# Kernel tuning notes

Hardware: AMD Instinct MI355X
Metric: run time of the kernel (lower is better)

Reference implementation:

```python
import jax, jax.numpy as jnp
import numpy as np

CHAMFER_W, NORMAL_W, EDGE_W, WATERTIGHT_W, SDF_W = 1.0, 0.5, 0.3, 0.2, 1.0
DIHEDRAL_THRESHOLD = 0.5
EPS_COS = 1e-8   # F.cosine_similarity eps
EPS_NRM = 1e-12  # F.normalize eps


def _pairwise_sqdist(p, g):
    # (B,N,3),(B,M,3) -> (B,N,M) squared distances, without (B,N,M,3) temp
    p2 = (p * p).sum(-1)
    g2 = (g * g).sum(-1)
    return p2[:, :, None] + g2[:, None, :] - 2.0 * jnp.einsum('bnd,bmd->bnm', p, g)


def _face_normals(verts, faces):
    v0, v1, v2 = verts[faces[:, 0]], verts[faces[:, 1]], verts[faces[:, 2]]
    n = jnp.cross(v1 - v0, v2 - v0)
    return n / jnp.maximum(jnp.linalg.norm(n, axis=-1, keepdims=True), EPS_NRM)


def _edge_structure(faces, num_verts):
    # All 3F directed edges (f_i, f_{(i+1)%3}), canonicalized to sorted keys.
    a = faces                      # (F,3)
    b = jnp.roll(faces, -1, axis=1)  # pairs (0,1),(1,2),(2,0)
    lo = jnp.minimum(a, b).reshape(-1)
    hi = jnp.maximum(a, b).reshape(-1)
    keys = lo * num_verts + hi      # unique int key per undirected edge (< 2^31)
    face_ids = jnp.repeat(jnp.arange(faces.shape[0], dtype=jnp.int32), 3)
    order = jnp.argsort(keys, stable=True)
    sk = keys[order]
    sf = face_ids[order]
    E = sk.shape[0]
    run_start = jnp.concatenate([jnp.array([True]), sk[1:] != sk[:-1]])
    eq_next = jnp.concatenate([sk[:-1] == sk[1:], jnp.array([False])])
    rs_pad = jnp.concatenate([run_start, jnp.array([True, True])])
    # pair2[i]: run of length exactly 2 starting at i -> faces sf[i], sf[i+1]
    pair2 = run_start & eq_next & rs_pad[2:]
    return sf, pair2, run_start


def _edge_sharpness(verts, faces):
    normals = _face_normals(verts, faces)
    sf, pair2, _ = _edge_structure(faces, verts.shape[0])
    sf_next = jnp.roll(sf, -1)
    cos = (normals[sf] * normals[sf_next]).sum(-1)
    terms = jax.nn.relu(cos - DIHEDRAL_THRESHOLD)
    cnt = pair2.sum()
    return jnp.where(cnt > 0, (terms * pair2).sum() / jnp.maximum(cnt, 1), 0.0)


def _watertight(faces, num_verts):
    _, pair2, run_start = _edge_structure(faces, num_verts)
    total = run_start.sum()
    bad = total - pair2.sum()
    return jnp.where(total > 0, bad.astype(jnp.float32) / jnp.maximum(total, 1).astype(jnp.float32), 0.0)


def setup_inputs():
    key = jax.random.key(0)
    ks = jax.random.split(key, 10)
    B, N, M, V, F, NS = 1, 8192, 8192, 20000, 40000, 65536
    return {
        'pred_sdf': jax.random.normal(ks[0], (B, NS, 1), jnp.float32),
        'gt_sdf': jax.random.normal(ks[1], (B, NS, 1), jnp.float32),
        'extracted_vertices': jax.random.normal(ks[2], (V, 3), jnp.float32),
        'extracted_faces': jax.random.randint(ks[3], (F, 3), 0, V, jnp.int32),
        'gt_vertices': jax.random.normal(ks[4], (V, 3), jnp.float32),
        'gt_faces': jax.random.randint(ks[5], (F, 3), 0, V, jnp.int32),
        'pred_points': jax.random.normal(ks[6], (B, N, 3), jnp.float32),
        'gt_points': jax.random.normal(ks[7], (B, M, 3), jnp.float32),
        'pred_normals': jax.random.normal(ks[8], (B, N, 3), jnp.float32),
        'gt_normals': jax.random.normal(ks[9], (B, M, 3), jnp.float32),
    }


def reference(pred_sdf, gt_sdf, extracted_vertices, extracted_faces, gt_vertices, gt_faces,
              pred_points, gt_points, pred_normals, gt_normals):
    # sdf supervision (L1)
    sdf_l = SDF_W * jnp.abs(pred_sdf - gt_sdf).mean()

    # chamfer
    dist = _pairwise_sqdist(pred_points, gt_points)  # (B,N,M)
    min_p2g = dist.min(axis=2).mean(axis=1)
    min_g2p = dist.min(axis=1).mean(axis=1)
    chamfer_l = CHAMFER_W * (min_p2g + min_g2p).mean()

    # normal consistency (nearest GT point per pred point)
    nn_idx = jnp.argmin(dist, axis=2)  # (B,N)
    matched = jnp.take_along_axis(gt_normals, nn_idx[..., None], axis=1)  # (B,N,3)
    pn = jnp.maximum(jnp.linalg.norm(pred_normals, axis=-1), EPS_COS)
    gn = jnp.maximum(jnp.linalg.norm(matched, axis=-1), EPS_COS)
    cos = (pred_normals * matched).sum(-1) / (pn * gn)
    normal_l = NORMAL_W * (1.0 - jnp.abs(cos)).mean()

    # edge sharpness (GT mesh args are unused by the original implementation)
    edge_l = EDGE_W * _edge_sharpness(extracted_vertices, extracted_faces)

    # watertight regularization
    wt_l = WATERTIGHT_W * _watertight(extracted_faces, extracted_vertices.shape[0])

    total = sdf_l + chamfer_l + normal_l + edge_l + wt_l
    return sdf_l, chamfer_l, normal_l, edge_l, wt_l, total
```

## Files before the change

### kernel.cpp

```cpp
#include <hip/hip_runtime.h>
#include <math.h>

#define TILE 128
#define REG 8
#define APB (256 * REG)
#define HASH_C 262144
#define HASH_MASK (HASH_C - 1)
#define EMPTY_SLOT 0xFFFFFFFFu
#define KEY_MASK ((1u << 29) - 1)
#define CNT_ONE (1u << 29)
#define SDF_BLOCKS 32

#define SBIAS 256.0f
#define TOPBITS 0x42000000u
#define PADW 480.0f


__device__ inline float waveReduceF(float v) {
#pragma unroll
  for (int off = 32; off > 0; off >>= 1) v += __shfl_down(v, off, 64);
  return v;
}

__global__ __launch_bounds__(256) void fused_kernel(
    const float* __restrict__ P, const float* __restrict__ G, int N, int M,
    int p2gBlocks, int chamferBlocks, int meshBlocks, int nTileG, int nTileP,
    unsigned long long* __restrict__ p2g, unsigned* __restrict__ g2p,
    const float* __restrict__ verts, const int* __restrict__ faces, int F, int V,
    float4* __restrict__ fn, unsigned* __restrict__ slots,
    unsigned* __restrict__ face0, unsigned* __restrict__ face1,
    unsigned* __restrict__ cnt, unsigned* __restrict__ pairList,
    const float* __restrict__ sdfA, const float* __restrict__ sdfB, int NS,
    float* __restrict__ sdfPartial, float* accumF, unsigned* accumU) {
  __shared__ float4 tile[TILE];
  __shared__ float shS[4];
  int tid = threadIdx.x;

  if (blockIdx.x == 0 && tid == 0) {
#pragma unroll
    for (int q = 0; q < 5; q++) accumF[q] = 0.f;
    accumU[0] = 0u;
  }

  if ((int)blockIdx.x >= chamferBlocks + meshBlocks) {
    int sb = blockIdx.x - chamferBlocks - meshBlocks;
    int t = sb * 256 + tid;
    int strideS = SDF_BLOCKS * 256;
    float ss = 0.f;
    for (int i = t; i < NS; i += strideS) ss += fabsf(sdfA[i] - sdfB[i]);
    ss = waveReduceF(ss);
    int lane = tid & 63, wid = tid >> 6;
    if (lane == 0) shS[wid] = ss;
    __syncthreads();
    if (tid == 0) sdfPartial[sb] = shS[0] + shS[1] + shS[2] + shS[3];
    return;
  }

  if ((int)blockIdx.x >= chamferBlocks) {
    int e = (blockIdx.x - chamferBlocks) * 256 + tid;
    bool valid = (e < 3 * F);
    unsigned c = 0xFFu;
    if (valid) {
      int f = e / 3, k = e - 3 * f;
      int a = faces[3 * f + k];
      int b = faces[3 * f + ((k + 1) % 3)];
      if (k == 0) {
        int i1 = faces[3 * f + 1], i2 = faces[3 * f + 2];
        float ax = verts[3 * a], ay = verts[3 * a + 1], az = verts[3 * a + 2];
        float bx = verts[3 * i1] - ax, by = verts[3 * i1 + 1] - ay, bz = verts[3 * i1 + 2] - az;
        float cx = verts[3 * i2] - ax, cy = verts[3 * i2 + 1] - ay, cz = verts[3 * i2 + 2] - az;
        float nx = by * cz - bz * cy;
        float ny = bz * cx - bx * cz;
        float nz = bx * cy - by * cx;
        float l = sqrtf(nx * nx + ny * ny + nz * nz);
        float inv = 1.f / fmaxf(l, 1e-12f);
        fn[f] = make_float4(nx * inv, ny * inv, nz * inv, 0.f);
      }
      unsigned lo = (unsigned)min(a, b), hi = (unsigned)max(a, b);
      unsigned key = lo * (unsigned)V + hi + 1u;
      unsigned h = (key * 2654435761u) & HASH_MASK;
      for (;;) {
        unsigned prev = atomicCAS(&slots[h], EMPTY_SLOT, key | CNT_ONE);
        if (prev == EMPTY_SLOT) { c = 0u; break; }
        if ((prev & KEY_MASK) == key) {
          c = (atomicAdd(&slots[h], CNT_ONE) >> 29) & 7u;
          break;
        }
        h = (h + 1) & HASH_MASK;
      }
      if (c == 0u) face0[h] = (unsigned)f;
      else if (c == 1u) {
        face1[h] = (unsigned)f;
        unsigned idx = atomicAdd(&cnt[2], 1u) + 1u;
        pairList[idx] = h;
      }
    }
    unsigned long long b0 = __ballot(valid && c == 0u);
    unsigned long long b1 = __ballot(valid && c == 1u);
    unsigned long long b2 = __ballot(valid && c == 2u);
    if ((tid & 63) == 0) {
      unsigned d = (unsigned)__popcll(b0);
      unsigned pd = (unsigned)__popcll(b1) - (unsigned)__popcll(b2);
      if (d) atomicAdd(&cnt[0], d);
      if (pd) atomicAdd(&cnt[1], pd);
    }
    return;
  }

  bool isP2G = ((int)blockIdx.x < p2gBlocks);
  const float* A;
  const float* B;
  int nA, nB, chunk, tileIdx;
  if (isP2G) {
    chunk = blockIdx.x / nTileG;
    tileIdx = blockIdx.x % nTileG;
    A = P; nA = N; B = G; nB = M;
  } else {
    int bid = blockIdx.x - p2gBlocks;
    chunk = bid / nTileP;
    tileIdx = bid % nTileP;
    A = G; nA = M; B = P; nB = N;
  }

  int abase = chunk * APB + tid;
  float px[REG], py[REG], pz[REG];
#pragma unroll
  for (int r = 0; r < REG; r++) {
    int i = abase + 256 * r;
    if (i < nA) { px[r] = A[3 * i]; py[r] = A[3 * i + 1]; pz[r] = A[3 * i + 2]; }
    else        { px[r] = 0.f; py[r] = 0.f; pz[r] = 0.f; }
  }

  int tbase = tileIdx * TILE;
  if (tid < TILE) {
    int j = tbase + tid;
    float4 v;
    if (j < nB) {
      float x = B[3 * j], y = B[3 * j + 1], z = B[3 * j + 2];
      v = make_float4(x, y, z, fmaf(0.5f, x * x + y * y + z * z, SBIAS));
    } else {
      v = make_float4(0.f, 0.f, 0.f, PADW);
    }
    tile[tid] = v;
  }
  __syncthreads();

  if (isP2G) {
    unsigned best[REG];
#pragma unroll
    for (int r = 0; r < REG; r++) best[r] = 0xFFFFFFFFu;
#pragma unroll 2
    for (int j = 0; j < TILE; j += 2) {
      float4 g0 = tile[j];
      float4 g1 = tile[j + 1];
#pragma unroll
      for (int r = 0; r < REG; r++) {
        float s0 = fmaf(-pz[r], g0.z, fmaf(-py[r], g0.y, fmaf(-px[r], g0.x, g0.w)));
        float s1 = fmaf(-pz[r], g1.z, fmaf(-py[r], g1.y, fmaf(-px[r], g1.x, g1.w)));
        unsigned k0 = (__float_as_uint(s0) << 7) | (unsigned)j;
        unsigned k1 = (__float_as_uint(s1) << 7) | (unsigned)(j + 1);
        best[r] = min(best[r], min(k0, k1));
      }
    }
#pragma unroll
    for (int r = 0; r < REG; r++) {
      int i = abase + 256 * r;
      if (i < nA) {
        unsigned sbits = (best[r] >> 7) | TOPBITS;
        unsigned idx = (unsigned)tbase + (best[r] & 127u);
        unsigned long long packed = ((unsigned long long)sbits << 32) | idx;
        atomicMin(&p2g[i], packed);
      }
    }
  } else {
    float best[REG];
#pragma unroll
    for (int r = 0; r < REG; r++) best[r] = INFINITY;
#pragma unroll 2
    for (int j = 0; j < TILE; j += 2) {
      float4 g0 = tile[j];
      float4 g1 = tile[j + 1];
#pragma unroll
      for (int r = 0; r < REG; r++) {
        float s0 = fmaf(-pz[r], g0.z, fmaf(-py[r], g0.y, fmaf(-px[r], g0.x, g0.w)));
        float s1 = fmaf(-pz[r], g1.z, fmaf(-py[r], g1.y, fmaf(-px[r], g1.x, g1.w)));
        best[r] = fminf(best[r], fminf(s0, s1));
      }
    }
#pragma unroll
    for (int r = 0; r < REG; r++) {
      int i = abase + 256 * r;
      if (i < nA) atomicMin(&g2p[i], __float_as_uint(best[r]));
    }
  }
}

__global__ __launch_bounds__(256) void finalize_kernel(
    const float* __restrict__ P, const float* __restrict__ G,
    const float* __restrict__ PN, const float* __restrict__ GN,
    const float* __restrict__ sdfPartial,
    const unsigned* __restrict__ slots, const unsigned* __restrict__ face0,
    const unsigned* __restrict__ face1, const float4* __restrict__ fn,
    const unsigned* __restrict__ cnt, const unsigned* __restrict__ pairList,
    int N, int M, int NS, int nBlocks,
    const unsigned long long* __restrict__ p2g, const unsigned* __restrict__ g2p,
    float* accumF, unsigned* accumU, float* out) {
  __shared__ float sh[20];
  int t = blockIdx.x * 256 + threadIdx.x;
  int stride = nBlocks * 256;
  float sp = 0.f, sg = 0.f, sn = 0.f, ss = 0.f, term = 0.f;
  if (t < N) {
    unsigned long long pk = p2g[t];
    float sprime = __uint_as_float((unsigned)(pk >> 32));
    int idx = (int)(pk & 0xFFFFFFFFull);
    float px = P[3 * t], py = P[3 * t + 1], pz = P[3 * t + 2];
    sp = px * px + py * py + pz * pz + 2.f * sprime - 2.f * SBIAS;
    float nx = PN[3 * t], ny = PN[3 * t + 1], nz = PN[3 * t + 2];
    float mx = GN[3 * idx], my = GN[3 * idx + 1], mz = GN[3 * idx + 2];
    float pn = fmaxf(sqrtf(nx * nx + ny * ny + nz * nz), 1e-8f);
    float gn = fmaxf(sqrtf(mx * mx + my * my + mz * mz), 1e-8f);
    float cosv = (nx * mx + ny * my + nz * mz) / (pn * gn);
    sn = 1.f - fabsf(cosv);
  }
  if (t < M) {
    float sprime = __uint_as_float(g2p[t]);
    float gx = G[3 * t], gy = G[3 * t + 1], gz = G[3 * t + 2];
    sg = gx * gx + gy * gy + gz * gz + 2.f * sprime - 2.f * SBIAS;
  }
  if (t < SDF_BLOCKS) ss = sdfPartial[t];
  unsigned listLen = cnt[2] + 1u;
  for (unsigned i = (unsigned)t; i < listLen; i += (unsigned)stride) {
    unsigned h = pairList[i];
    if ((slots[h] >> 29) == 2u) {
      float4 n0 = fn[face0[h]];
      float4 n1 = fn[face1[h]];
      float c = n0.x * n1.x + n0.y * n1.y + n0.z * n1.z;
      term += fmaxf(c - 0.5f, 0.f);
    }
  }
  sp = waveReduceF(sp);
  sg = waveReduceF(sg);
  sn = waveReduceF(sn);
  ss = waveReduceF(ss);
  term = waveReduceF(term);
  int lane = threadIdx.x & 63, wid = threadIdx.x >> 6;
  if (lane == 0) {
    sh[wid] = sp; sh[4 + wid] = sg; sh[8 + wid] = sn; sh[12 + wid] = ss;
    sh[16 + wid] = term;
  }
  __syncthreads();
  if (threadIdx.x == 0) {
    atomicAdd(&accumF[1], sh[0] + sh[1] + sh[2] + sh[3]);
    atomicAdd(&accumF[2], sh[4] + sh[5] + sh[6] + sh[7]);
    atomicAdd(&accumF[3], sh[8] + sh[9] + sh[10] + sh[11]);
    atomicAdd(&accumF[0], sh[12] + sh[13] + sh[14] + sh[15]);
    atomicAdd(&accumF[4], sh[16] + sh[17] + sh[18] + sh[19]);
    __threadfence();
    unsigned ticket = atomicAdd(&accumU[0], 1u);
    if (ticket == (unsigned)(nBlocks - 1)) {
      float a0 = atomicAdd(&accumF[0], 0.f);
      float a1 = atomicAdd(&accumF[1], 0.f);
      float a2 = atomicAdd(&accumF[2], 0.f);
      float a3 = atomicAdd(&accumF[3], 0.f);
      float a4 = atomicAdd(&accumF[4], 0.f);
      float runsF = (float)(cnt[0] + 1u);
      float pairsF = (float)(cnt[1] + 1u);
      float sdf = a0 / (float)NS;
      float chamfer = a1 / (float)N + a2 / (float)M;
      float normal = 0.5f * (a3 / (float)N);
      float edge = (pairsF > 0.f) ? 0.3f * (a4 / pairsF) : 0.f;
      float wt = (runsF > 0.f) ? 0.2f * ((runsF - pairsF) / runsF) : 0.f;
      out[0] = sdf;
      out[1] = chamfer;
      out[2] = normal;
      out[3] = edge;
      out[4] = wt;
      out[5] = sdf + chamfer + normal + edge + wt;
    }
  }
}

extern "C" void kernel_launch(void* const* d_in, const int* in_sizes, int n_in,
                              void* d_out, int out_size, void* d_ws,
                              size_t ws_size, hipStream_t stream) {
  const float* pred_sdf = (const float*)d_in[0];
  const float* gt_sdf   = (const float*)d_in[1];
  const float* ev       = (const float*)d_in[2];
  const int*   ef       = (const int*)d_in[3];
  const float* pp       = (const float*)d_in[6];
  const float* gp       = (const float*)d_in[7];
  const float* pn       = (const float*)d_in[8];
  const float* gn       = (const float*)d_in[9];
  int NS = in_sizes[0];
  int V = in_sizes[2] / 3;
  int F = in_sizes[3] / 3;
  int N = in_sizes[6] / 3;
  int M = in_sizes[7] / 3;
  float* out = (float*)d_out;

  char* ws = (char*)d_ws;
  size_t offSlots = 0;
  size_t offP2G = offSlots + (size_t)HASH_C * 4;
  size_t offG2P = offP2G + (size_t)N * 8;
  size_t offCnt = offG2P + (size_t)M * 4;
  size_t ffBytes = offCnt + 16;
  size_t offAccumF = (ffBytes + 63) & ~(size_t)63;
  size_t offAccumU = offAccumF + 32;
  size_t offFace0 = offAccumU + 32;
  size_t offFace1 = offFace0 + (size_t)HASH_C * 4;
  size_t offFN = (offFace1 + (size_t)HASH_C * 4 + 15) & ~(size_t)15;
  size_t offPairList = offFN + (size_t)F * 16;
  size_t offSdfP = offPairList + (size_t)(3 * F) * 4;

  unsigned* slots = (unsigned*)(ws + offSlots);
  unsigned long long* p2gArr = (unsigned long long*)(ws + offP2G);
  unsigned* g2pArr = (unsigned*)(ws + offG2P);
  unsigned* cnt = (unsigned*)(ws + offCnt);
  float* accumF = (float*)(ws + offAccumF);
  unsigned* accumU = (unsigned*)(ws + offAccumU);
  unsigned* face0 = (unsigned*)(ws + offFace0);
  unsigned* face1 = (unsigned*)(ws + offFace1);
  float4* fnorm = (float4*)(ws + offFN);
  unsigned* pairList = (unsigned*)(ws + offPairList);
  float* sdfPartial = (float*)(ws + offSdfP);

  hipMemsetAsync(ws, 0xFF, ffBytes, stream);

  int nChunkP = (N + APB - 1) / APB, nTileG = (M + TILE - 1) / TILE;
  int nChunkG = (M + APB - 1) / APB, nTileP = (N + TILE - 1) / TILE;
  int p2gBlocks = nChunkP * nTileG;
  int chamferBlocks = p2gBlocks + nChunkG * nTileP;
  int meshBlocks = (3 * F + 255) / 256;
  fused_kernel<<<chamferBlocks + meshBlocks + SDF_BLOCKS, 256, 0, stream>>>(
      pp, gp, N, M, p2gBlocks, chamferBlocks, meshBlocks, nTileG, nTileP,
      p2gArr, g2pArr, ev, ef, F, V, fnorm, slots, face0, face1, cnt, pairList,
      pred_sdf, gt_sdf, NS, sdfPartial, accumF, accumU);

  int mx = (N > M ? N : M);
  int nFin = (mx + 255) / 256;
  if (nFin < 64) nFin = 64;
  finalize_kernel<<<nFin, 256, 0, stream>>>(
      pp, gp, pn, gn, sdfPartial, slots, face0, face1, fnorm,
      cnt, pairList, N, M, NS, nFin, p2gArr, g2pArr, accumF, accumU, out);
}
```

Measured before the change: 117.0 us.

## Replace chamfer atomicMin with per-tile partial buffers reduced in finalize

Each chamfer block now writes its per-point tile minimum to a dedicated slot in a (tiles × points) partial buffer instead of doing global atomicMin. The finalize kernel scans all tiles per point and reconstructs the packed distance/index minimum. This removes atomic contention and the memset of the p2g/g2p arrays. In exchange it adds workspace traffic proportional to tiles × points and serial loops in finalize.

```diff
diff --git a/kernel.cpp b/kernel.cpp
--- a/kernel.cpp
+++ b/kernel.cpp
@@ -25,7 +25,7 @@
 __global__ __launch_bounds__(256) void fused_kernel(
     const float* __restrict__ P, const float* __restrict__ G, int N, int M,
     int p2gBlocks, int chamferBlocks, int meshBlocks, int nTileG, int nTileP,
-    unsigned long long* __restrict__ p2g, unsigned* __restrict__ g2p,
+    unsigned* __restrict__ p2gPart, unsigned* __restrict__ g2pPart,
     const float* __restrict__ verts, const int* __restrict__ faces, int F, int V,
     float4* __restrict__ fn, unsigned* __restrict__ slots,
     unsigned* __restrict__ face0, unsigned* __restrict__ face1,
@@ -165,12 +165,7 @@
 #pragma unroll
     for (int r = 0; r < REG; r++) {
       int i = abase + 256 * r;
-      if (i < nA) {
-        unsigned sbits = (best[r] >> 7) | TOPBITS;
-        unsigned idx = (unsigned)tbase + (best[r] & 127u);
-        unsigned long long packed = ((unsigned long long)sbits << 32) | idx;
-        atomicMin(&p2g[i], packed);
-      }
+      if (i < nA) p2gPart[(size_t)tileIdx * N + i] = best[r];
     }
   } else {
     float best[REG];
@@ -190,7 +185,7 @@
 #pragma unroll
     for (int r = 0; r < REG; r++) {
       int i = abase + 256 * r;
-      if (i < nA) atomicMin(&g2p[i], __float_as_uint(best[r]));
+      if (i < nA) g2pPart[(size_t)tileIdx * M + i] = __float_as_uint(best[r]);
     }
   }
 }
@@ -202,17 +197,24 @@
     const unsigned* __restrict__ slots, const unsigned* __restrict__ face0,
     const unsigned* __restrict__ face1, const float4* __restrict__ fn,
     const unsigned* __restrict__ cnt, const unsigned* __restrict__ pairList,
-    int N, int M, int NS, int nBlocks,
-    const unsigned long long* __restrict__ p2g, const unsigned* __restrict__ g2p,
+    int N, int M, int NS, int nBlocks, int nTileG, int nTileP,
+    const unsigned* __restrict__ p2gPart, const unsigned* __restrict__ g2pPart,
     float* accumF, unsigned* accumU, float* out) {
   __shared__ float sh[20];
   int t = blockIdx.x * 256 + threadIdx.x;
   int stride = nBlocks * 256;
   float sp = 0.f, sg = 0.f, sn = 0.f, ss = 0.f, term = 0.f;
   if (t < N) {
-    unsigned long long pk = p2g[t];
-    float sprime = __uint_as_float((unsigned)(pk >> 32));
-    int idx = (int)(pk & 0xFFFFFFFFull);
+    unsigned long long cand = 0xFFFFFFFFFFFFFFFFull;
+#pragma unroll 8
+    for (int k = 0; k < nTileG; k++) {
+      unsigned b = p2gPart[(size_t)k * N + t];
+      unsigned long long c2 =
+          ((unsigned long long)(b >> 7) << 32) | (unsigned)(k * TILE + (int)(b & 127u));
+      cand = min(cand, c2);
+    }
+    float sprime = __uint_as_float(((unsigned)(cand >> 32)) | TOPBITS);
+    int idx = (int)(cand & 0xFFFFFFFFull);
     float px = P[3 * t], py = P[3 * t + 1], pz = P[3 * t + 2];
     sp = px * px + py * py + pz * pz + 2.f * sprime - 2.f * SBIAS;
     float nx = PN[3 * t], ny = PN[3 * t + 1], nz = PN[3 * t + 2];
@@ -223,7 +225,10 @@
     sn = 1.f - fabsf(cosv);
   }
   if (t < M) {
-    float sprime = __uint_as_float(g2p[t]);
+    unsigned vb = 0xFFFFFFFFu;
+#pragma unroll 8
+    for (int k = 0; k < nTileP; k++) vb = min(vb, g2pPart[(size_t)k * M + t]);
+    float sprime = __uint_as_float(vb);
     float gx = G[3 * t], gy = G[3 * t + 1], gz = G[3 * t + 2];
     sg = gx * gx + gy * gy + gz * gz + 2.f * sprime - 2.f * SBIAS;
   }
@@ -298,11 +303,12 @@
   int M = in_sizes[7] / 3;
   float* out = (float*)d_out;
 
+  int nChunkP = (N + APB - 1) / APB, nTileG = (M + TILE - 1) / TILE;
+  int nChunkG = (M + APB - 1) / APB, nTileP = (N + TILE - 1) / TILE;
+
   char* ws = (char*)d_ws;
   size_t offSlots = 0;
-  size_t offP2G = offSlots + (size_t)HASH_C * 4;
-  size_t offG2P = offP2G + (size_t)N * 8;
-  size_t offCnt = offG2P + (size_t)M * 4;
+  size_t offCnt = offSlots + (size_t)HASH_C * 4;
   size_t ffBytes = offCnt + 16;
   size_t offAccumF = (ffBytes + 63) & ~(size_t)63;
   size_t offAccumU = offAccumF + 32;
@@ -311,10 +317,10 @@
   size_t offFN = (offFace1 + (size_t)HASH_C * 4 + 15) & ~(size_t)15;
   size_t offPairList = offFN + (size_t)F * 16;
   size_t offSdfP = offPairList + (size_t)(3 * F) * 4;
+  size_t offP2GP = (offSdfP + (size_t)SDF_BLOCKS * 4 + 63) & ~(size_t)63;
+  size_t offG2PP = offP2GP + (size_t)nTileG * N * 4;
 
   unsigned* slots = (unsigned*)(ws + offSlots);
-  unsigned long long* p2gArr = (unsigned long long*)(ws + offP2G);
-  unsigned* g2pArr = (unsigned*)(ws + offG2P);
   unsigned* cnt = (unsigned*)(ws + offCnt);
   float* accumF = (float*)(ws + offAccumF);
   unsigned* accumU = (unsigned*)(ws + offAccumU);
@@ -323,17 +329,17 @@
   float4* fnorm = (float4*)(ws + offFN);
   unsigned* pairList = (unsigned*)(ws + offPairList);
   float* sdfPartial = (float*)(ws + offSdfP);
+  unsigned* p2gPart = (unsigned*)(ws + offP2GP);
+  unsigned* g2pPart = (unsigned*)(ws + offG2PP);
 
   hipMemsetAsync(ws, 0xFF, ffBytes, stream);
 
-  int nChunkP = (N + APB - 1) / APB, nTileG = (M + TILE - 1) / TILE;
-  int nChunkG = (M + APB - 1) / APB, nTileP = (N + TILE - 1) / TILE;
   int p2gBlocks = nChunkP * nTileG;
   int chamferBlocks = p2gBlocks + nChunkG * nTileP;
   int meshBlocks = (3 * F + 255) / 256;
   fused_kernel<<<chamferBlocks + meshBlocks + SDF_BLOCKS, 256, 0, stream>>>(
       pp, gp, N, M, p2gBlocks, chamferBlocks, meshBlocks, nTileG, nTileP,
-      p2gArr, g2pArr, ev, ef, F, V, fnorm, slots, face0, face1, cnt, pairList,
+      p2gPart, g2pPart, ev, ef, F, V, fnorm, slots, face0, face1, cnt, pairList,
       pred_sdf, gt_sdf, NS, sdfPartial, accumF, accumU);
 
   int mx = (N > M ? N : M);
@@ -341,5 +347,6 @@
   if (nFin < 64) nFin = 64;
   finalize_kernel<<<nFin, 256, 0, stream>>>(
       pp, gp, pn, gn, sdfPartial, slots, face0, face1, fnorm,
-      cnt, pairList, N, M, NS, nFin, p2gArr, g2pArr, accumF, accumU, out);
+      cnt, pairList, N, M, NS, nFin, nTileG, nTileP, p2gPart, g2pPart,
+      accumF, accumU, out);
 }
```

Measured after the change: 122.8 us. 5.0% more time.

## Compute both chamfer directions in one pass over each distance tile

Applied to the files above, without the earlier changes.

Before, two separate block sets each evaluated every pred-GT pair, one for pred-to-GT and one for GT-to-pred. Now each block evaluates each pair once and takes the minimum along both axes. The GT-side minimum comes from a per-wave shuffle reduction plus a shared-memory combine across the four waves, followed by one atomicMin per GT point. This halves the chamfer block count and the pair work, but adds per-pair fmas for the second score and a 6-step shuffle reduction on every pair of columns.

```diff
diff --git a/kernel.cpp b/kernel.cpp
--- a/kernel.cpp
+++ b/kernel.cpp
@@ -14,6 +14,7 @@
 #define SBIAS 256.0f
 #define TOPBITS 0x42000000u
 #define PADW 480.0f
+#define BIGS 1e9f
 
 
 __device__ inline float waveReduceF(float v) {
@@ -24,7 +25,7 @@
 
 __global__ __launch_bounds__(256) void fused_kernel(
     const float* __restrict__ P, const float* __restrict__ G, int N, int M,
-    int p2gBlocks, int chamferBlocks, int meshBlocks, int nTileG, int nTileP,
+    int chamferBlocks, int meshBlocks, int nTileG,
     unsigned long long* __restrict__ p2g, unsigned* __restrict__ g2p,
     const float* __restrict__ verts, const int* __restrict__ faces, int F, int V,
     float4* __restrict__ fn, unsigned* __restrict__ slots,
@@ -33,6 +34,7 @@
     const float* __restrict__ sdfA, const float* __restrict__ sdfB, int NS,
     float* __restrict__ sdfPartial, float* accumF, unsigned* accumU) {
   __shared__ float4 tile[TILE];
+  __shared__ float waveG[4][TILE];
   __shared__ float shS[4];
   int tid = threadIdx.x;
 
@@ -107,36 +109,28 @@
     return;
   }
 
-  bool isP2G = ((int)blockIdx.x < p2gBlocks);
-  const float* A;
-  const float* B;
-  int nA, nB, chunk, tileIdx;
-  if (isP2G) {
-    chunk = blockIdx.x / nTileG;
-    tileIdx = blockIdx.x % nTileG;
-    A = P; nA = N; B = G; nB = M;
-  } else {
-    int bid = blockIdx.x - p2gBlocks;
-    chunk = bid / nTileP;
-    tileIdx = bid % nTileP;
-    A = G; nA = M; B = P; nB = N;
-  }
+  int chunk = blockIdx.x / nTileG;
+  int tileIdx = blockIdx.x % nTileG;
 
   int abase = chunk * APB + tid;
-  float px[REG], py[REG], pz[REG];
+  float px[REG], py[REG], pz[REG], pw[REG];
 #pragma unroll
   for (int r = 0; r < REG; r++) {
     int i = abase + 256 * r;
-    if (i < nA) { px[r] = A[3 * i]; py[r] = A[3 * i + 1]; pz[r] = A[3 * i + 2]; }
-    else        { px[r] = 0.f; py[r] = 0.f; pz[r] = 0.f; }
+    if (i < N) {
+      px[r] = P[3 * i]; py[r] = P[3 * i + 1]; pz[r] = P[3 * i + 2];
+      pw[r] = fmaf(0.5f, px[r] * px[r] + py[r] * py[r] + pz[r] * pz[r], SBIAS);
+    } else {
+      px[r] = 0.f; py[r] = 0.f; pz[r] = 0.f; pw[r] = BIGS;
+    }
   }
 
   int tbase = tileIdx * TILE;
   if (tid < TILE) {
     int j = tbase + tid;
     float4 v;
-    if (j < nB) {
-      float x = B[3 * j], y = B[3 * j + 1], z = B[3 * j + 2];
+    if (j < M) {
+      float x = G[3 * j], y = G[3 * j + 1], z = G[3 * j + 2];
       v = make_float4(x, y, z, fmaf(0.5f, x * x + y * y + z * z, SBIAS));
     } else {
       v = make_float4(0.f, 0.f, 0.f, PADW);
@@ -145,52 +139,52 @@
   }
   __syncthreads();
 
-  if (isP2G) {
-    unsigned best[REG];
-#pragma unroll
-    for (int r = 0; r < REG; r++) best[r] = 0xFFFFFFFFu;
+  int lane = tid & 63, wid = tid >> 6;
+  unsigned best[REG];
+#pragma unroll
+  for (int r = 0; r < REG; r++) best[r] = 0xFFFFFFFFu;
 #pragma unroll 2
-    for (int j = 0; j < TILE; j += 2) {
-      float4 g0 = tile[j];
-      float4 g1 = tile[j + 1];
-#pragma unroll
-      for (int r = 0; r < REG; r++) {
-        float s0 = fmaf(-pz[r], g0.z, fmaf(-py[r], g0.y, fmaf(-px[r], g0.x, g0.w)));
-        float s1 = fmaf(-pz[r], g1.z, fmaf(-py[r], g1.y, fmaf(-px[r], g1.x, g1.w)));
-        unsigned k0 = (__float_as_uint(s0) << 7) | (unsigned)j;
-        unsigned k1 = (__float_as_uint(s1) << 7) | (unsigned)(j + 1);
-        best[r] = min(best[r], min(k0, k1));
-      }
-    }
+  for (int j = 0; j < TILE; j += 2) {
+    float4 g0 = tile[j];
+    float4 g1 = tile[j + 1];
+    float m0 = BIGS, m1 = BIGS;
 #pragma unroll
     for (int r = 0; r < REG; r++) {
-      int i = abase + 256 * r;
-      if (i < nA) {
-        unsigned sbits = (best[r] >> 7) | TOPBITS;
-        unsigned idx = (unsigned)tbase + (best[r] & 127u);
-        unsigned long long packed = ((unsigned long long)sbits << 32) | idx;
-        atomicMin(&p2g[i], packed);
-      }
-    }
-  } else {
-    float best[REG];
-#pragma unroll
-    for (int r = 0; r < REG; r++) best[r] = INFINITY;
-#pragma unroll 2
-    for (int j = 0; j < TILE; j += 2) {
-      float4 g0 = tile[j];
-      float4 g1 = tile[j + 1];
-#pragma unroll
-      for (int r = 0; r < REG; r++) {
-        float s0 = fmaf(-pz[r], g0.z, fmaf(-py[r], g0.y, fmaf(-px[r], g0.x, g0.w)));
-        float s1 = fmaf(-pz[r], g1.z, fmaf(-py[r], g1.y, fmaf(-px[r], g1.x, g1.w)));
-        best[r] = fminf(best[r], fminf(s0, s1));
-      }
-    }
-#pragma unroll
-    for (int r = 0; r < REG; r++) {
-      int i = abase + 256 * r;
-      if (i < nA) atomicMin(&g2p[i], __float_as_uint(best[r]));
+      float s0 = fmaf(-pz[r], g0.z, fmaf(-py[r], g0.y, fmaf(-px[r], g0.x, g0.w)));
+      float s1 = fmaf(-pz[r], g1.z, fmaf(-py[r], g1.y, fmaf(-px[r], g1.x, g1.w)));
+      unsigned k0 = (__float_as_uint(s0) << 7) | (unsigned)j;
+      unsigned k1 = (__float_as_uint(s1) << 7) | (unsigned)(j + 1);
+      best[r] = min(best[r], min(k0, k1));
+      float t0 = fmaf(-g0.z, pz[r], fmaf(-g0.y, py[r], fmaf(-g0.x, px[r], pw[r])));
+      float t1 = fmaf(-g1.z, pz[r], fmaf(-g1.y, py[r], fmaf(-g1.x, px[r], pw[r])));
+      m0 = fminf(m0, t0);
+      m1 = fminf(m1, t1);
+    }
+#pragma unroll
+    for (int off = 32; off > 0; off >>= 1) {
+      m0 = fminf(m0, __shfl_down(m0, off, 64));
+      m1 = fminf(m1, __shfl_down(m1, off, 64));
+    }
+    if (lane == 0) { waveG[wid][j] = m0; waveG[wid][j + 1] = m1; }
+  }
+
+#pragma unroll
+  for (int r = 0; r < REG; r++) {
+    int i = abase + 256 * r;
+    if (i < N) {
+      unsigned sbits = (best[r] >> 7) | TOPBITS;
+      unsigned idx = (unsigned)tbase + (best[r] & 127u);
+      unsigned long long packed = ((unsigned long long)sbits << 32) | idx;
+      atomicMin(&p2g[i], packed);
+    }
+  }
+  __syncthreads();
+  if (tid < TILE) {
+    int j = tbase + tid;
+    if (j < M) {
+      float v = fminf(fminf(waveG[0][tid], waveG[1][tid]),
+                      fminf(waveG[2][tid], waveG[3][tid]));
+      atomicMin(&g2p[j], __float_as_uint(v));
     }
   }
 }
@@ -326,13 +320,12 @@
 
   hipMemsetAsync(ws, 0xFF, ffBytes, stream);
 
-  int nChunkP = (N + APB - 1) / APB, nTileG = (M + TILE - 1) / TILE;
-  int nChunkG = (M + APB - 1) / APB, nTileP = (N + TILE - 1) / TILE;
-  int p2gBlocks = nChunkP * nTileG;
-  int chamferBlocks = p2gBlocks + nChunkG * nTileP;
+  int nChunkP = (N + APB - 1) / APB;
+  int nTileG = (M + TILE - 1) / TILE;
+  int chamferBlocks = nChunkP * nTileG;
   int meshBlocks = (3 * F + 255) / 256;
   fused_kernel<<<chamferBlocks + meshBlocks + SDF_BLOCKS, 256, 0, stream>>>(
-      pp, gp, N, M, p2gBlocks, chamferBlocks, meshBlocks, nTileG, nTileP,
+      pp, gp, N, M, chamferBlocks, meshBlocks, nTileG,
       p2gArr, g2pArr, ev, ef, F, V, fnorm, slots, face0, face1, cnt, pairList,
       pred_sdf, gt_sdf, NS, sdfPartial, accumF, accumU);
 
```

Measured after the change: 141.8 us. 1.21x slower.
